# Optimization experiments

Hardware: AMD Instinct MI355X
Metric: run time of the kernel (lower is better)

The kernel has to match this reference:

```python
import jax, jax.numpy as jnp
import numpy as np

N, E, D, H, L, G = 20000, 320000, 128, 3, 3, 64
NEG_SLOPE = 0.2


def _seg_softmax(x, seg, num_segments):
    # x: [E, ...] logits, seg: [E] int segment ids. Softmax within each segment.
    m = jax.ops.segment_max(x, seg, num_segments=num_segments)
    e = jnp.exp(x - m[seg])  # m[seg] is finite wherever an edge exists
    s = jax.ops.segment_sum(e, seg, num_segments=num_segments)
    return e / s[seg]


def _gat_layer(feat, src, dst, fc_w, a_ns, a_nd, trans_w, trans_b):
    # feat: [N, D]; fc_w: [H*D, D]; a_ns/a_nd: [H, D]; trans_w: [D, H*D]
    h = (feat @ fc_w.T).reshape(N, H, D)                      # [N, H, D]
    s_ns = jnp.einsum('nhd,hd->nh', h, a_ns)                  # [N, H]
    s_nd = jnp.einsum('nhd,hd->nh', h, a_nd)                  # [N, H]
    e = jax.nn.leaky_relu(s_ns[src] + s_nd[dst], NEG_SLOPE)   # [E, H]
    a = _seg_softmax(e, dst, N)                               # edge softmax per dst
    msg = h[src] * a[:, :, None]                              # [E, H, D]
    agg = jax.ops.segment_sum(msg, dst, num_segments=N)       # [N, H, D]
    return agg.reshape(N, H * D) @ trans_w.T + trans_b        # [N, D]


def _attn_pool(feat, gid, p1_w, p1_b, p2_w, p2_b):
    # GlobalAttentionPooling: gate MLP -> softmax over nodes per graph -> weighted sum
    gate = jax.nn.relu(feat @ p1_w.T + p1_b) @ p2_w.T + p2_b  # [N, 1]
    alpha = _seg_softmax(gate[:, 0], gid, G)[:, None]         # [N, 1]
    return jax.ops.segment_sum(alpha * feat, gid, num_segments=G)  # [G, D]


def setup_inputs() -> dict:
    key = jax.random.key(0)
    ks = jax.random.split(key, 16)
    feat = jax.random.normal(ks[0], (N, D), dtype=jnp.float32)
    src = jax.random.randint(ks[1], (E,), 0, N, dtype=jnp.int32)
    dst = jax.random.randint(ks[2], (E,), 0, N, dtype=jnp.int32)
    node_gid = jnp.sort(jax.random.randint(ks[3], (N,), 0, G, dtype=jnp.int32))
    sc = 0.05
    return {
        'feat': feat, 'src': src, 'dst': dst, 'node_gid': node_gid,
        'fc_w': jax.random.normal(ks[4], (L, H * D, D), dtype=jnp.float32) * sc,
        'a_ns': jax.random.normal(ks[5], (L, H, D), dtype=jnp.float32) * sc,
        'a_nd': jax.random.normal(ks[6], (L, H, D), dtype=jnp.float32) * sc,
        'trans_w': jax.random.normal(ks[7], (L, D, H * D), dtype=jnp.float32) * sc,
        'trans_b': jax.random.normal(ks[8], (L, D), dtype=jnp.float32) * sc,
        'p1_w': jax.random.normal(ks[9], (L, 2 * D, D), dtype=jnp.float32) * sc,
        'p1_b': jax.random.normal(ks[10], (L, 2 * D), dtype=jnp.float32) * sc,
        'p2_w': jax.random.normal(ks[11], (L, 1, 2 * D), dtype=jnp.float32) * sc,
        'p2_b': jax.random.normal(ks[12], (L, 1), dtype=jnp.float32) * sc,
    }


def reference(feat, src, dst, node_gid, fc_w, a_ns, a_nd, trans_w, trans_b,
              p1_w, p1_b, p2_w, p2_b):
    # MLAPModel.forward with res=True, vir=False, dropout off (eval), Tflag=0
    graph_embs = []
    for d in range(L):
        feat_in = feat
        feat = _gat_layer(feat, src, dst, fc_w[d], a_ns[d], a_nd[d],
                          trans_w[d], trans_b[d])
        if d < L - 1:
            feat = jax.nn.relu(feat)
        feat = feat + feat_in  # residual
        graph_embs.append(_attn_pool(feat, node_gid, p1_w[d], p1_b[d],
                                     p2_w[d], p2_b[d]))
    return jnp.stack(graph_embs, axis=0).mean(axis=0)  # [G, D]
```

## Files before the change

kernel.cpp:

```cpp
#include <hip/hip_runtime.h>
#include <hip/hip_bf16.h>

#define N_NODES 20000
#define N_EDGES 320000
#define DIM 128
#define HEADS 3
#define LAYERS 3
#define NGRAPH 64
#define NEG_SLOPE 0.2f
#define NODE_BLOCKS ((N_NODES + 63) / 64)
#define NBLK32 ((N_NODES + 31) / 32)

typedef const __hip_bfloat16* bfp;
typedef __hip_bfloat16 bf16;
typedef short v8s __attribute__((ext_vector_type(8)));
typedef float v4f __attribute__((ext_vector_type(4)));

#define GLD_LDS(gp, lp) \
    __builtin_amdgcn_global_load_lds( \
        (const __attribute__((address_space(1))) void*)(gp), \
        (__attribute__((address_space(3))) void*)(lp), 16, 0, 0)

__device__ __forceinline__ float b2f(unsigned short u) {
    return __uint_as_float(((unsigned)u) << 16);
}
__device__ __forceinline__ float lo2f(unsigned u) { return __uint_as_float(u << 16); }
__device__ __forceinline__ float hi2f(unsigned u) { return __uint_as_float(u & 0xffff0000u); }
__device__ __forceinline__ float leaky(float z) {
    return z >= 0.f ? z : NEG_SLOPE * z;
}
__device__ __forceinline__ unsigned packbf(float a, float b) {
    bf16 x = __float2bfloat16(a), y = __float2bfloat16(b);
    return (unsigned)*(unsigned short*)&x | ((unsigned)*(unsigned short*)&y << 16);
}
__device__ __forceinline__ unsigned short f2bfbits(float v) {
    bf16 x = __float2bfloat16(v);
    return *(unsigned short*)&x;
}

__device__ __forceinline__ void stage_swz(const short* base, int t0, int K,
                                          int k0, short* lds, int gidx) {
    int row = gidx >> 2, pos = gidx & 3;
    int kch = pos ^ ((row >> 1) & 3);
    GLD_LDS(base + (size_t)(t0 + row) * K + k0 + kch * 8, lds + gidx * 8);
}
__device__ __forceinline__ v8s fragx(const short* lds, int R, int q) {
    int g = R * 4 + (q ^ ((R >> 1) & 3));
    return *(const v8s*)(lds + g * 8);
}

__device__ __forceinline__ void stage_panelB(const short* base, int t0, int K,
                                             int k0, short* lds, int tid) {
#pragma unroll
    for (int j = 0; j < 8; ++j) {
        int g = j * 256 + tid;
        stage_swz(base, t0, K, k0 + (g >> 9) * 32, lds + (g >> 9) * 4096, g & 511);
    }
}
__device__ __forceinline__ void stage_panelA32(const short* base, int t0, int K,
                                               int k0, short* lds, int tid) {
#pragma unroll
    for (int j = 0; j < 2; ++j) {
        int g = j * 256 + tid;
        stage_swz(base, t0, K, k0 + (g >> 7) * 32, lds + (g >> 7) * 1024, g & 127);
    }
}

__global__ void init_kernel(unsigned* __restrict__ z, int nzd,
                            const unsigned short* __restrict__ probe,
                            int* __restrict__ dflag) {
    int gid = blockIdx.x * 256 + threadIdx.x;
    for (int i = gid; i < nzd; i += gridDim.x * 256) z[i] = 0u;
    if (blockIdx.x == 0) {
        int c = 0;
#pragma unroll
        for (int j = 0; j < 64; ++j) {
            unsigned short u = probe[threadIdx.x * 64 + j];
            c += (((u >> 7) & 0xFF) >= 140) ? 1 : 0;
        }
        for (int o = 32; o > 0; o >>= 1) c += __shfl_down(c, o);
        __shared__ int r[4];
        if ((threadIdx.x & 63) == 0) r[threadIdx.x >> 6] = c;
        __syncthreads();
        if (threadIdx.x == 0) *dflag = r[0] + r[1] + r[2] + r[3];
    }
}

#define NCVT 9
struct CvtArgs {
    const void* src[NCVT];
    bf16* dst[NCVT];
    int n4[NCVT];
    int n[NCVT];
};
__global__ void cvtcount_kernel(CvtArgs args, const int* __restrict__ flag,
                                const int* __restrict__ dst, int* __restrict__ deg,
                                int cvtBlocks) {
    if ((int)blockIdx.x >= cvtBlocks) {
        int e = (blockIdx.x - cvtBlocks) * 256 + threadIdx.x;
        if (e < N_EDGES) atomicAdd(&deg[dst[e]], 1);
        return;
    }
    int i = blockIdx.x * 256 + threadIdx.x;
    int f = (*flag) > 8;
#pragma unroll
    for (int s = 0; s < NCVT; ++s) {
        int ns4 = args.n4[s];
        if (i < ns4) {
            int ns = args.n[s];
            int base = i * 4;
            bf16* dstp = args.dst[s];
            if (f) {
                const float* sp = (const float*)args.src[s];
                if (base + 3 < ns) {
                    float4 v = *(const float4*)(sp + base);
                    ushort4 pk = { f2bfbits(v.x), f2bfbits(v.y),
                                   f2bfbits(v.z), f2bfbits(v.w) };
                    *(ushort4*)(dstp + base) = pk;
                } else {
                    for (int j = 0; j < 4 && base + j < ns; ++j)
                        dstp[base + j] = __float2bfloat16(sp[base + j]);
                }
            } else {
                const bf16* sp = (const bf16*)args.src[s];
                if (base + 3 < ns) {
                    *(ushort4*)(dstp + base) = *(const ushort4*)(sp + base);
                } else {
                    for (int j = 0; j < 4 && base + j < ns; ++j)
                        dstp[base + j] = sp[base + j];
                }
            }
            return;
        }
        i -= ns4;
    }
}

__global__ void sentinel_kernel(bf16* out, int n) {
    int i = blockIdx.x * 256 + threadIdx.x;
    if (i < n) out[i] = __float2bfloat16(2.0f);
}

__global__ __launch_bounds__(256) void scanprep_kernel(
    const int* __restrict__ cnt, int* __restrict__ ptr,
    const int* __restrict__ gid, int* __restrict__ gptr,
    const bf16* __restrict__ cfc, const bf16* __restrict__ cans,
    const bf16* __restrict__ cand, const bf16* __restrict__ ctw,
    bf16* __restrict__ mcat, float* __restrict__ vcat)
{
    int tid = threadIdx.x;
    if ((int)blockIdx.x < LAYERS * 25) {
        const int l = blockIdx.x / 25;
        const int b = blockIdx.x % 25;
        const bf16* fc = cfc + (size_t)l * 384 * 128;
        if (b < 24) {
            const int h = b >> 3, kc = b & 7;
            const bf16* tw = ctw + (size_t)l * 128 * 384;
            bf16* mc = mcat + (size_t)l * 128 * 384;
            const int d = tid & 127;
            const int kh = tid >> 7;
            const int k0 = kc * 16 + kh * 8;
            float acc[8] = {0.f, 0.f, 0.f, 0.f, 0.f, 0.f, 0.f, 0.f};
            for (int j = 0; j < 128; ++j) {
                float w = __bfloat162float(tw[(size_t)d * 384 + h * 128 + j]);
                v8s fv = *(const v8s*)(fc + (size_t)(h * 128 + j) * 128 + k0);
#pragma unroll
                for (int i = 0; i < 8; ++i)
                    acc[i] += w * b2f((unsigned short)fv[i]);
            }
            v8s ov;
#pragma unroll
            for (int i = 0; i < 8; ++i) ov[i] = (short)f2bfbits(acc[i]);
            *(v8s*)(mc + (size_t)d * 384 + h * 128 + k0) = ov;
        } else {
            const int k = tid & 127;
            const int grp = tid >> 7;
            const bf16* av = (grp ? cand : cans) + (size_t)l * 384;
            float a0 = 0.f, a1 = 0.f, a2 = 0.f;
            for (int j = 0; j < 128; ++j) {
                a0 += __bfloat162float(av[j])       * __bfloat162float(fc[(size_t)j * 128 + k]);
                a1 += __bfloat162float(av[128 + j]) * __bfloat162float(fc[(size_t)(128 + j) * 128 + k]);
                a2 += __bfloat162float(av[256 + j]) * __bfloat162float(fc[(size_t)(256 + j) * 128 + k]);
            }
            float* vc = vcat + (size_t)l * 6 * 128;
            vc[(grp * 3 + 0) * 128 + k] = a0;
            vc[(grp * 3 + 1) * 128 + k] = a1;
            vc[(grp * 3 + 2) * 128 + k] = a2;
        }
        return;
    }
    if (tid <= NGRAPH) {
        int lo = 0, hi = N_NODES;
        while (lo < hi) {
            int mid = (lo + hi) >> 1;
            if (gid[mid] < tid) lo = mid + 1; else hi = mid;
        }
        gptr[tid] = lo;
    }
    const int chunk = (N_NODES + 255) / 256;
    int b = tid * chunk, e = min(b + chunk, N_NODES);
    int loc = 0;
    for (int i = b; i < e; ++i) loc += cnt[i];
    int lane = tid & 63, wv = tid >> 6;
    int v = loc;
#pragma unroll
    for (int o = 1; o < 64; o <<= 1) {
        int t = __shfl_up(v, o);
        if (lane >= o) v += t;
    }
    __shared__ int wsum[4];
    if (lane == 63) wsum[wv] = v;
    __syncthreads();
    int wo = 0;
    for (int j = 0; j < wv; ++j) wo += wsum[j];
    int run = wo + v - loc;
    if (tid == 255) ptr[N_NODES] = wsum[0] + wsum[1] + wsum[2] + wsum[3];
    for (int i = b; i < e; ++i) { ptr[i] = run; run += cnt[i]; }
}

__device__ __forceinline__ void score_block(
    const unsigned* __restrict__ featdw, const float* __restrict__ vc,
    float* __restrict__ s_all, int blk, int tid)
{
    const int wv = tid >> 6, lane = tid & 63;
    float2 vv0 = *(const float2*)(vc + 0 * 128 + lane * 2);
    float2 vv1 = *(const float2*)(vc + 1 * 128 + lane * 2);
    float2 vv2 = *(const float2*)(vc + 2 * 128 + lane * 2);
    float2 vv3 = *(const float2*)(vc + 3 * 128 + lane * 2);
    float2 vv4 = *(const float2*)(vc + 4 * 128 + lane * 2);
    float2 vv5 = *(const float2*)(vc + 5 * 128 + lane * 2);
    const int nbase = blk * 64 + wv * 16;
#pragma unroll 1
    for (int t = 0; t < 16; ++t) {
        const int n = nbase + t;
        if (n >= N_NODES) return;
        unsigned u = featdw[(size_t)n * 64 + lane];
        float lo = lo2f(u), hi = hi2f(u);
        float p0 = lo * vv0.x + hi * vv0.y;
        float p1 = lo * vv1.x + hi * vv1.y;
        float p2 = lo * vv2.x + hi * vv2.y;
        float p3 = lo * vv3.x + hi * vv3.y;
        float p4 = lo * vv4.x + hi * vv4.y;
        float p5 = lo * vv5.x + hi * vv5.y;
#pragma unroll
        for (int o = 1; o < 64; o <<= 1) {
            p0 += __shfl_xor(p0, o); p1 += __shfl_xor(p1, o);
            p2 += __shfl_xor(p2, o); p3 += __shfl_xor(p3, o);
            p4 += __shfl_xor(p4, o); p5 += __shfl_xor(p5, o);
        }
        float outv = p0;
        outv = (lane == 1) ? p1 : outv;
        outv = (lane == 2) ? p2 : outv;
        outv = (lane == 4) ? p3 : outv;
        outv = (lane == 5) ? p4 : outv;
        outv = (lane == 6) ? p5 : outv;
        if (lane < 7 && lane != 3)
            s_all[(size_t)n * 8 + lane] = outv;
    }
}

__global__ __launch_bounds__(256) void fillscore_kernel(
    const bf16* __restrict__ pfeat,
    const float* __restrict__ vc, float* __restrict__ s_all,
    const int* __restrict__ src, const int* __restrict__ dst,
    const int* __restrict__ rp, int* __restrict__ cursor,
    int* __restrict__ esrc, int fillBlocks)
{
    const int tid = threadIdx.x;
    if ((int)blockIdx.x < fillBlocks) {
        int e = blockIdx.x * 256 + tid;
        if (e < N_EDGES) {
            int d = dst[e];
            int pos = rp[d] + atomicAdd(&cursor[d], 1);
            esrc[pos] = src[e];
        }
        return;
    }
    score_block((const unsigned*)pfeat, vc, s_all, blockIdx.x - fillBlocks, tid);
}

__global__ __launch_bounds__(256) void aggpool_kernel(
    const unsigned* __restrict__ featdw, const int* __restrict__ rp,
    const int* __restrict__ esrc, const float* __restrict__ s_all,
    bf16* __restrict__ aggF, const float* __restrict__ gp,
    const int* __restrict__ gptr, float* __restrict__ out_acc,
    int poolBlocks)
{
    __shared__ float4 pv[4][64];
    __shared__ float red[4];
    const int tid = threadIdx.x;
    if ((int)blockIdx.x < poolBlocks) {
        const bf16* pfeat = (const bf16*)featdw;
        const int g = blockIdx.x >> 3;
        const int chunk = blockIdx.x & 7;
        const int beg = gptr[g], end = gptr[g + 1];
        if (beg >= end) return;
        float m = -1e30f;
        for (int i = beg + tid; i < end; i += 256)
            m = fmaxf(m, gp[i]);
#pragma unroll
        for (int o = 32; o > 0; o >>= 1) m = fmaxf(m, __shfl_xor(m, o));
        if ((tid & 63) == 0) red[tid >> 6] = m;
        __syncthreads();
        m = fmaxf(fmaxf(red[0], red[1]), fmaxf(red[2], red[3]));
        __syncthreads();
        float s = 0.f;
        for (int i = beg + tid; i < end; i += 256)
            s += __expf(gp[i] - m);
#pragma unroll
        for (int o = 32; o > 0; o >>= 1) s += __shfl_xor(s, o);
        if ((tid & 63) == 0) red[tid >> 6] = s;
        __syncthreads();
        float inv = 1.f / (red[0] + red[1] + red[2] + red[3]);
        const int p = tid >> 7;
        const int c = tid & 127;
        float acc = 0.f;
        for (int i = beg + chunk * 2 + p; i < end; i += 16) {
            float w = __expf(gp[i] - m);
            acc += w * __bfloat162float(pfeat[(size_t)i * DIM + c]);
        }
        acc *= inv;
        atomicAdd(&out_acc[g * DIM + c], acc);
        return;
    }
    const int wv = tid >> 6;
    const int lane = tid & 63;
    const int node = (blockIdx.x - poolBlocks) * 4 + wv;
    if (node >= N_NODES) return;
    const int beg = rp[node], end = rp[node + 1];
    const int cnt = end - beg;
    unsigned* outp = (unsigned*)(aggF + (size_t)node * (HEADS * DIM));
    if (cnt <= 0) {
        outp[lane] = 0u; outp[64 + lane] = 0u; outp[128 + lane] = 0u;
        return;
    }
    const float nd0 = s_all[(size_t)node * 8 + 4];
    const float nd1 = s_all[(size_t)node * 8 + 5];
    const float nd2 = s_all[(size_t)node * 8 + 6];
    float sl0 = 0.f, sl1 = 0.f, sl2 = 0.f;
    float a00 = 0.f, a01 = 0.f, a10 = 0.f, a11 = 0.f, a20 = 0.f, a21 = 0.f;
    for (int c0 = 0; c0 < cnt; c0 += 64) {
        const int ce = min(64, cnt - c0);
        if (lane < ce) {
            int s = esrc[beg + c0 + lane];
            float4 q = *(const float4*)(s_all + (size_t)s * 8);
            float4 r;
            r.x = __expf(leaky(q.x + nd0));
            r.y = __expf(leaky(q.y + nd1));
            r.z = __expf(leaky(q.z + nd2));
            r.w = __int_as_float(s);
            sl0 += r.x; sl1 += r.y; sl2 += r.z;
            pv[wv][lane] = r;
        }
#pragma unroll 8
        for (int j = 0; j < ce; ++j) {
            float4 e = pv[wv][j];
            int s = __float_as_int(e.w);
            unsigned u = featdw[(size_t)s * 64 + lane];
            float lo = lo2f(u), hi = hi2f(u);
            a00 += e.x * lo; a01 += e.x * hi;
            a10 += e.y * lo; a11 += e.y * hi;
            a20 += e.z * lo; a21 += e.z * hi;
        }
    }
#pragma unroll
    for (int o = 1; o < 64; o <<= 1) {
        sl0 += __shfl_xor(sl0, o);
        sl1 += __shfl_xor(sl1, o);
        sl2 += __shfl_xor(sl2, o);
    }
    const float i0 = 1.f / sl0, i1 = 1.f / sl1, i2 = 1.f / sl2;
    outp[lane]       = packbf(a00 * i0, a01 * i0);
    outp[64 + lane]  = packbf(a10 * i1, a11 * i1);
    outp[128 + lane] = packbf(a20 * i2, a21 * i2);
}

__global__ __launch_bounds__(256) void fusedgemm_kernel(
    const bf16* __restrict__ A, const bf16* __restrict__ B,
    bf16* __restrict__ C, const bf16* __restrict__ bias,
    const bf16* __restrict__ resid, int do_relu,
    const bf16* __restrict__ p1w, const bf16* __restrict__ p1b,
    const bf16* __restrict__ p2w, float* __restrict__ gpart,
    const float* __restrict__ vc_next, float* __restrict__ s_next)
{
    __shared__ short lsA[4096];
    __shared__ short lsB[16384];
    __shared__ float sred[2][32][8];
    const int tid = threadIdx.x;
    const int wv = tid >> 6, lane = tid & 63;
    const int quad = lane >> 4, r16 = lane & 15;
    const int rw = wv & 1, cg = wv >> 1;
    const int m0 = blockIdx.x * 32;
    const short* As = (const short*)A;
    const short* Bs = (const short*)B;

    v4f acc[4];
#pragma unroll
    for (int t = 0; t < 4; ++t) acc[t] = (v4f){0.f, 0.f, 0.f, 0.f};

#pragma unroll
    for (int ks = 0; ks < 3; ++ks) {
        const int k0 = ks * 128;
        stage_panelA32(As, m0, 384, k0, lsA, tid);
        stage_panelB(Bs, 0, 384, k0, lsB, tid);
        __syncthreads();
#pragma unroll
        for (int c = 0; c < 4; ++c) {
            v8s a = fragx(lsA + c * 1024, rw * 16 + r16, quad);
#pragma unroll
            for (int t = 0; t < 4; ++t) {
                v8s b = fragx(lsB + c * 4096, cg * 64 + t * 16 + r16, quad);
                acc[t] = __builtin_amdgcn_mfma_f32_16x16x32_bf16(a, b, acc[t], 0, 0, 0);
            }
        }
        __syncthreads();
    }

    float bbv[4];
#pragma unroll
    for (int t = 0; t < 4; ++t)
        bbv[t] = __bfloat162float(bias[cg * 64 + t * 16 + r16]);
    float s0[4], s1[4], s2[4], s3[4], s4[4], s5[4];
#pragma unroll
    for (int reg = 0; reg < 4; ++reg) {
        s0[reg] = 0.f; s1[reg] = 0.f; s2[reg] = 0.f;
        s3[reg] = 0.f; s4[reg] = 0.f; s5[reg] = 0.f;
    }
#pragma unroll
    for (int t = 0; t < 4; ++t) {
        const int n = cg * 64 + t * 16 + r16;
        float v0 = vc_next ? vc_next[0 * 128 + n] : 0.f;
        float v1 = vc_next ? vc_next[1 * 128 + n] : 0.f;
        float v2 = vc_next ? vc_next[2 * 128 + n] : 0.f;
        float v3 = vc_next ? vc_next[3 * 128 + n] : 0.f;
        float v4 = vc_next ? vc_next[4 * 128 + n] : 0.f;
        float v5 = vc_next ? vc_next[5 * 128 + n] : 0.f;
        const int cch = n >> 5, nc = n & 31, qq = nc >> 3, e = nc & 7;
#pragma unroll
        for (int reg = 0; reg < 4; ++reg) {
            const int R = rw * 16 + quad * 4 + reg;
            const int m = m0 + R;
            float v = acc[t][reg] + bbv[t];
            if (do_relu) v = fmaxf(v, 0.f);
            v += __bfloat162float(resid[(size_t)m * 128 + n]);
            C[(size_t)m * 128 + n] = __float2bfloat16(v);
            const int pos = qq ^ ((R >> 1) & 3);
            lsA[cch * 1024 + (R * 4 + pos) * 8 + e] = (short)f2bfbits(v);
            s0[reg] += v * v0; s1[reg] += v * v1; s2[reg] += v * v2;
            s3[reg] += v * v3; s4[reg] += v * v4; s5[reg] += v * v5;
        }
    }
    if (vc_next) {
#pragma unroll
        for (int reg = 0; reg < 4; ++reg) {
#pragma unroll
            for (int o = 1; o < 16; o <<= 1) {
                s0[reg] += __shfl_xor(s0[reg], o);
                s1[reg] += __shfl_xor(s1[reg], o);
                s2[reg] += __shfl_xor(s2[reg], o);
                s3[reg] += __shfl_xor(s3[reg], o);
                s4[reg] += __shfl_xor(s4[reg], o);
                s5[reg] += __shfl_xor(s5[reg], o);
            }
            if (r16 == 0) {
                const int R = rw * 16 + quad * 4 + reg;
                sred[cg][R][0] = s0[reg]; sred[cg][R][1] = s1[reg];
                sred[cg][R][2] = s2[reg]; sred[cg][R][3] = s3[reg];
                sred[cg][R][4] = s4[reg]; sred[cg][R][5] = s5[reg];
            }
        }
    }
    __syncthreads();
    if (vc_next && tid < 192) {
        const int R = tid / 6, c = tid - R * 6;
        const float sv = sred[0][R][c] + sred[1][R][c];
        s_next[(size_t)(m0 + R) * 8 + (c < 3 ? c : c + 1)] = sv;
    }

    float gacc[4] = {0.f, 0.f, 0.f, 0.f};
#pragma unroll 1
    for (int hh = 0; hh < 2; ++hh) {
        if (hh) __syncthreads();
        stage_panelB((const short*)p1w, hh * 128, 128, 0, lsB, tid);
        __syncthreads();
        v4f a2[4];
#pragma unroll
        for (int t = 0; t < 4; ++t) a2[t] = (v4f){0.f, 0.f, 0.f, 0.f};
#pragma unroll
        for (int c = 0; c < 4; ++c) {
            v8s a = fragx(lsA + c * 1024, rw * 16 + r16, quad);
#pragma unroll
            for (int t = 0; t < 4; ++t) {
                v8s b = fragx(lsB + c * 4096, cg * 64 + t * 16 + r16, quad);
                a2[t] = __builtin_amdgcn_mfma_f32_16x16x32_bf16(a, b, a2[t], 0, 0, 0);
            }
        }
#pragma unroll
        for (int t = 0; t < 4; ++t) {
            const int n = hh * 128 + cg * 64 + t * 16 + r16;
            float b1 = __bfloat162float(p1b[n]);
            float pw = __bfloat162float(p2w[n]);
#pragma unroll
            for (int reg = 0; reg < 4; ++reg)
                gacc[reg] += fmaxf(a2[t][reg] + b1, 0.f) * pw;
        }
    }
#pragma unroll
    for (int reg = 0; reg < 4; ++reg) {
#pragma unroll
        for (int o = 1; o < 16; o <<= 1) gacc[reg] += __shfl_xor(gacc[reg], o);
        if (r16 == 0) sred[cg][rw * 16 + quad * 4 + reg][6] = gacc[reg];
    }
    __syncthreads();
    if (tid < 32) gpart[m0 + tid] = sred[0][tid][6] + sred[1][tid][6];
}

__global__ void __launch_bounds__(256) pool_acc(
    const bf16* __restrict__ feat, const float* __restrict__ gp,
    const int* __restrict__ gptr, float* __restrict__ out_acc)
{
    const int g = blockIdx.x;
    const int chunk = blockIdx.y;
    const int tid = threadIdx.x;
    const int beg = gptr[g], end = gptr[g + 1];
    if (beg >= end) return;
    __shared__ float red[4];
    float m = -1e30f;
    for (int i = beg + tid; i < end; i += 256)
        m = fmaxf(m, gp[i]);
#pragma unroll
    for (int o = 32; o > 0; o >>= 1) m = fmaxf(m, __shfl_xor(m, o));
    if ((tid & 63) == 0) red[tid >> 6] = m;
    __syncthreads();
    m = fmaxf(fmaxf(red[0], red[1]), fmaxf(red[2], red[3]));
    __syncthreads();
    float s = 0.f;
    for (int i = beg + tid; i < end; i += 256)
        s += __expf(gp[i] - m);
#pragma unroll
    for (int o = 32; o > 0; o >>= 1) s += __shfl_xor(s, o);
    if ((tid & 63) == 0) red[tid >> 6] = s;
    __syncthreads();
    float inv = 1.f / (red[0] + red[1] + red[2] + red[3]);
    const int p = tid >> 7;
    const int c = tid & 127;
    float acc = 0.f;
    for (int i = beg + chunk * 2 + p; i < end; i += 16) {
        float w = __expf(gp[i] - m);
        acc += w * __bfloat162float(feat[(size_t)i * DIM + c]);
    }
    acc *= inv;
    atomicAdd(&out_acc[g * DIM + c], acc);
}

__global__ void writeout_kernel(const float* __restrict__ out_acc,
                                void* __restrict__ out, const int* __restrict__ flag) {
    int i = blockIdx.x * 256 + threadIdx.x;
    if (i < NGRAPH * DIM) {
        float v = out_acc[i] * (1.f / 3.f);
        if ((*flag) > 8) ((float*)out)[i] = v;
        else ((bf16*)out)[i] = __float2bfloat16(v);
    }
}

extern "C" void kernel_launch(void* const* d_in, const int* in_sizes, int n_in,
                              void* d_out, int out_size, void* d_ws, size_t ws_size,
                              hipStream_t stream)
{
    const void* feat_in = d_in[0];
    const int* src = (const int*)d_in[1];
    const int* dst = (const int*)d_in[2];
    const int* gid = (const int*)d_in[3];

    char* base = (char*)d_ws;
    size_t off = 0;
    auto carve = [&](size_t bytes) -> void* {
        void* p = base + off;
        off = (off + bytes + 255) & ~(size_t)255;
        return p;
    };
    int* dflag = (int*)carve(256);
    size_t zbytes = sizeof(int) * 2 * N_NODES + sizeof(float) * NGRAPH * DIM;
    char* zreg  = (char*)carve(zbytes);
    int* deg    = (int*)zreg;
    int* cursor = deg + N_NODES;
    float* out_acc = (float*)(cursor + N_NODES);
    float* gpart3 = (float*)carve(sizeof(float) * LAYERS * N_NODES);
    int* rp     = (int*)carve(sizeof(int) * (N_NODES + 1));
    int* gptr   = (int*)carve(sizeof(int) * (NGRAPH + 1));
    int* esrc   = (int*)carve(sizeof(int) * N_EDGES);
    float* s_bufA = (float*)carve(sizeof(float) * N_NODES * 8);
    float* s_bufB = (float*)carve(sizeof(float) * N_NODES * 8);
    float* vcat = (float*)carve(sizeof(float) * LAYERS * 6 * 128);
    bf16* mcat  = (bf16*)carve(sizeof(bf16) * LAYERS * 128 * 384);
    bf16* featA = (bf16*)carve(sizeof(bf16) * N_NODES * DIM);
    bf16* featB = (bf16*)carve(sizeof(bf16) * N_NODES * DIM);
    bf16* cfc   = (bf16*)carve(sizeof(bf16) * LAYERS * HEADS * DIM * DIM);
    bf16* cans  = (bf16*)carve(sizeof(bf16) * LAYERS * HEADS * DIM);
    bf16* cand  = (bf16*)carve(sizeof(bf16) * LAYERS * HEADS * DIM);
    bf16* ctw   = (bf16*)carve(sizeof(bf16) * LAYERS * DIM * HEADS * DIM);
    bf16* ctb   = (bf16*)carve(sizeof(bf16) * LAYERS * DIM);
    bf16* cp1w  = (bf16*)carve(sizeof(bf16) * LAYERS * 2 * DIM * DIM);
    bf16* cp1b  = (bf16*)carve(sizeof(bf16) * LAYERS * 2 * DIM);
    bf16* cp2w  = (bf16*)carve(sizeof(bf16) * LAYERS * 2 * DIM);
    bf16* aggF  = (bf16*)carve(sizeof(bf16) * N_NODES * HEADS * DIM);
    carve(131072);

    if (off > ws_size) {
        sentinel_kernel<<<(out_size + 255) / 256, 256, 0, stream>>>(
            (bf16*)d_out, out_size);
        return;
    }

    init_kernel<<<128, 256, 0, stream>>>(
        (unsigned*)zreg, (int)(zbytes / 4), (const unsigned short*)feat_in, dflag);

    CvtArgs ca;
    const int cvt_n[NCVT] = {
        N_NODES * DIM, LAYERS * HEADS * DIM * DIM, LAYERS * HEADS * DIM,
        LAYERS * HEADS * DIM, LAYERS * DIM * HEADS * DIM, LAYERS * DIM,
        LAYERS * 2 * DIM * DIM, LAYERS * 2 * DIM, LAYERS * 2 * DIM };
    bf16* cvt_dst[NCVT] = { featA, cfc, cans, cand, ctw, ctb, cp1w, cp1b, cp2w };
    const int cvt_src_idx[NCVT] = { 0, 4, 5, 6, 7, 8, 9, 10, 11 };
    int total4 = 0;
    for (int s = 0; s < NCVT; ++s) {
        ca.src[s] = d_in[cvt_src_idx[s]];
        ca.dst[s] = cvt_dst[s];
        ca.n[s] = cvt_n[s];
        ca.n4[s] = (cvt_n[s] + 3) / 4;
        total4 += ca.n4[s];
    }
    const int cvtBlocks = (total4 + 255) / 256;
    const int cntBlocks = (N_EDGES + 255) / 256;
    cvtcount_kernel<<<cvtBlocks + cntBlocks, 256, 0, stream>>>(
        ca, dflag, dst, deg, cvtBlocks);

    scanprep_kernel<<<LAYERS * 25 + 1, 256, 0, stream>>>(
        deg, rp, gid, gptr, cfc, cans, cand, ctw, mcat, vcat);

    bf16* fin = featA;
    bf16* fout = featB;
    for (int d = 0; d < LAYERS; ++d) {
        float* s_cur = (d & 1) ? s_bufB : s_bufA;
        float* s_next = (d & 1) ? s_bufA : s_bufB;
        if (d == 0) {
            fillscore_kernel<<<cntBlocks + NODE_BLOCKS, 256, 0, stream>>>(
                fin, vcat, s_cur, src, dst, rp, cursor, esrc, cntBlocks);
        }
        const int poolBlocks = (d == 0) ? 0 : NGRAPH * 8;
        aggpool_kernel<<<poolBlocks + (N_NODES + 3) / 4, 256, 0, stream>>>(
            (const unsigned*)fin, rp, esrc, s_cur, aggF,
            (d == 0) ? nullptr : gpart3 + (size_t)(d - 1) * N_NODES,
            gptr, out_acc, poolBlocks);
        fusedgemm_kernel<<<NBLK32, 256, 0, stream>>>(
            aggF, mcat + (size_t)d * 128 * 384, fout,
            ctb + (size_t)d * DIM, fin, (d < LAYERS - 1) ? 1 : 0,
            cp1w + (size_t)d * 2 * DIM * DIM, cp1b + (size_t)d * 2 * DIM,
            cp2w + (size_t)d * 2 * DIM, gpart3 + (size_t)d * N_NODES,
            (d < LAYERS - 1) ? vcat + (size_t)(d + 1) * 6 * 128 : nullptr,
            s_next);
        bf16* t = fin; fin = fout; fout = t;
    }
    pool_acc<<<dim3(NGRAPH, 8), 256, 0, stream>>>(
        fin, gpart3 + (size_t)2 * N_NODES, gptr, out_acc);
    writeout_kernel<<<(NGRAPH * DIM + 255) / 256, 256, 0, stream>>>(
        out_acc, d_out, dflag);
}
```

Measured before the change: 295.2 us.

## Fuse setup kernels into one cooperative kernel and fold writeout into pool_acc

Replaces the four setup launches (init, convert/count, scan/prep, fill/score) with a single cooperative kernel that uses grid-wide syncs between phases. A fallback to the old kernels remains if the cooperative launch fails. The final writeout kernel is merged into pool_acc using a last-block-done counter. The aim is to cut launch gaps and kernel boundaries on a short pipeline. The cost is grid.sync overhead, and the setup phases now run on a fixed grid of 512 blocks.

```diff
diff --git a/kernel.cpp b/kernel.cpp
--- a/kernel.cpp
+++ b/kernel.cpp
@@ -1,5 +1,8 @@
 #include <hip/hip_runtime.h>
 #include <hip/hip_bf16.h>
+#include <hip/hip_cooperative_groups.h>
+
+namespace cg = cooperative_groups;
 
 #define N_NODES 20000
 #define N_EDGES 320000
@@ -66,26 +69,6 @@
     }
 }
 
-__global__ void init_kernel(unsigned* __restrict__ z, int nzd,
-                            const unsigned short* __restrict__ probe,
-                            int* __restrict__ dflag) {
-    int gid = blockIdx.x * 256 + threadIdx.x;
-    for (int i = gid; i < nzd; i += gridDim.x * 256) z[i] = 0u;
-    if (blockIdx.x == 0) {
-        int c = 0;
-#pragma unroll
-        for (int j = 0; j < 64; ++j) {
-            unsigned short u = probe[threadIdx.x * 64 + j];
-            c += (((u >> 7) & 0xFF) >= 140) ? 1 : 0;
-        }
-        for (int o = 32; o > 0; o >>= 1) c += __shfl_down(c, o);
-        __shared__ int r[4];
-        if ((threadIdx.x & 63) == 0) r[threadIdx.x >> 6] = c;
-        __syncthreads();
-        if (threadIdx.x == 0) *dflag = r[0] + r[1] + r[2] + r[3];
-    }
-}
-
 #define NCVT 9
 struct CvtArgs {
     const void* src[NCVT];
@@ -93,16 +76,7 @@
     int n4[NCVT];
     int n[NCVT];
 };
-__global__ void cvtcount_kernel(CvtArgs args, const int* __restrict__ flag,
-                                const int* __restrict__ dst, int* __restrict__ deg,
-                                int cvtBlocks) {
-    if ((int)blockIdx.x >= cvtBlocks) {
-        int e = (blockIdx.x - cvtBlocks) * 256 + threadIdx.x;
-        if (e < N_EDGES) atomicAdd(&deg[dst[e]], 1);
-        return;
-    }
-    int i = blockIdx.x * 256 + threadIdx.x;
-    int f = (*flag) > 8;
+__device__ __forceinline__ void cvt_item(const CvtArgs& args, int i, int f) {
 #pragma unroll
     for (int s = 0; s < NCVT; ++s) {
         int ns4 = args.n4[s];
@@ -136,88 +110,6 @@
     }
 }
 
-__global__ void sentinel_kernel(bf16* out, int n) {
-    int i = blockIdx.x * 256 + threadIdx.x;
-    if (i < n) out[i] = __float2bfloat16(2.0f);
-}
-
-__global__ __launch_bounds__(256) void scanprep_kernel(
-    const int* __restrict__ cnt, int* __restrict__ ptr,
-    const int* __restrict__ gid, int* __restrict__ gptr,
-    const bf16* __restrict__ cfc, const bf16* __restrict__ cans,
-    const bf16* __restrict__ cand, const bf16* __restrict__ ctw,
-    bf16* __restrict__ mcat, float* __restrict__ vcat)
-{
-    int tid = threadIdx.x;
-    if ((int)blockIdx.x < LAYERS * 25) {
-        const int l = blockIdx.x / 25;
-        const int b = blockIdx.x % 25;
-        const bf16* fc = cfc + (size_t)l * 384 * 128;
-        if (b < 24) {
-            const int h = b >> 3, kc = b & 7;
-            const bf16* tw = ctw + (size_t)l * 128 * 384;
-            bf16* mc = mcat + (size_t)l * 128 * 384;
-            const int d = tid & 127;
-            const int kh = tid >> 7;
-            const int k0 = kc * 16 + kh * 8;
-            float acc[8] = {0.f, 0.f, 0.f, 0.f, 0.f, 0.f, 0.f, 0.f};
-            for (int j = 0; j < 128; ++j) {
-                float w = __bfloat162float(tw[(size_t)d * 384 + h * 128 + j]);
-                v8s fv = *(const v8s*)(fc + (size_t)(h * 128 + j) * 128 + k0);
-#pragma unroll
-                for (int i = 0; i < 8; ++i)
-                    acc[i] += w * b2f((unsigned short)fv[i]);
-            }
-            v8s ov;
-#pragma unroll
-            for (int i = 0; i < 8; ++i) ov[i] = (short)f2bfbits(acc[i]);
-            *(v8s*)(mc + (size_t)d * 384 + h * 128 + k0) = ov;
-        } else {
-            const int k = tid & 127;
-            const int grp = tid >> 7;
-            const bf16* av = (grp ? cand : cans) + (size_t)l * 384;
-            float a0 = 0.f, a1 = 0.f, a2 = 0.f;
-            for (int j = 0; j < 128; ++j) {
-                a0 += __bfloat162float(av[j])       * __bfloat162float(fc[(size_t)j * 128 + k]);
-                a1 += __bfloat162float(av[128 + j]) * __bfloat162float(fc[(size_t)(128 + j) * 128 + k]);
-                a2 += __bfloat162float(av[256 + j]) * __bfloat162float(fc[(size_t)(256 + j) * 128 + k]);
-            }
-            float* vc = vcat + (size_t)l * 6 * 128;
-            vc[(grp * 3 + 0) * 128 + k] = a0;
-            vc[(grp * 3 + 1) * 128 + k] = a1;
-            vc[(grp * 3 + 2) * 128 + k] = a2;
-        }
-        return;
-    }
-    if (tid <= NGRAPH) {
-        int lo = 0, hi = N_NODES;
-        while (lo < hi) {
-            int mid = (lo + hi) >> 1;
-            if (gid[mid] < tid) lo = mid + 1; else hi = mid;
-        }
-        gptr[tid] = lo;
-    }
-    const int chunk = (N_NODES + 255) / 256;
-    int b = tid * chunk, e = min(b + chunk, N_NODES);
-    int loc = 0;
-    for (int i = b; i < e; ++i) loc += cnt[i];
-    int lane = tid & 63, wv = tid >> 6;
-    int v = loc;
-#pragma unroll
-    for (int o = 1; o < 64; o <<= 1) {
-        int t = __shfl_up(v, o);
-        if (lane >= o) v += t;
-    }
-    __shared__ int wsum[4];
-    if (lane == 63) wsum[wv] = v;
-    __syncthreads();
-    int wo = 0;
-    for (int j = 0; j < wv; ++j) wo += wsum[j];
-    int run = wo + v - loc;
-    if (tid == 255) ptr[N_NODES] = wsum[0] + wsum[1] + wsum[2] + wsum[3];
-    for (int i = b; i < e; ++i) { ptr[i] = run; run += cnt[i]; }
-}
-
 __device__ __forceinline__ void score_block(
     const unsigned* __restrict__ featdw, const float* __restrict__ vc,
     float* __restrict__ s_all, int blk, int tid)
@@ -259,6 +151,184 @@
     }
 }
 
+__device__ __forceinline__ void prep_body(
+    int pb, int tid, const bf16* __restrict__ cfc,
+    const bf16* __restrict__ cans, const bf16* __restrict__ cand,
+    const bf16* __restrict__ ctw, bf16* __restrict__ mcat,
+    float* __restrict__ vcat)
+{
+    const int l = pb / 25;
+    const int b = pb % 25;
+    const bf16* fc = cfc + (size_t)l * 384 * 128;
+    if (b < 24) {
+        const int h = b >> 3, kc = b & 7;
+        const bf16* tw = ctw + (size_t)l * 128 * 384;
+        bf16* mc = mcat + (size_t)l * 128 * 384;
+        const int d = tid & 127;
+        const int kh = tid >> 7;
+        const int k0 = kc * 16 + kh * 8;
+        float acc[8] = {0.f, 0.f, 0.f, 0.f, 0.f, 0.f, 0.f, 0.f};
+        for (int j = 0; j < 128; ++j) {
+            float w = __bfloat162float(tw[(size_t)d * 384 + h * 128 + j]);
+            v8s fv = *(const v8s*)(fc + (size_t)(h * 128 + j) * 128 + k0);
+#pragma unroll
+            for (int i = 0; i < 8; ++i)
+                acc[i] += w * b2f((unsigned short)fv[i]);
+        }
+        v8s ov;
+#pragma unroll
+        for (int i = 0; i < 8; ++i) ov[i] = (short)f2bfbits(acc[i]);
+        *(v8s*)(mc + (size_t)d * 384 + h * 128 + k0) = ov;
+    } else {
+        const int k = tid & 127;
+        const int grp = tid >> 7;
+        const bf16* av = (grp ? cand : cans) + (size_t)l * 384;
+        float a0 = 0.f, a1 = 0.f, a2 = 0.f;
+        for (int j = 0; j < 128; ++j) {
+            a0 += __bfloat162float(av[j])       * __bfloat162float(fc[(size_t)j * 128 + k]);
+            a1 += __bfloat162float(av[128 + j]) * __bfloat162float(fc[(size_t)(128 + j) * 128 + k]);
+            a2 += __bfloat162float(av[256 + j]) * __bfloat162float(fc[(size_t)(256 + j) * 128 + k]);
+        }
+        float* vc = vcat + (size_t)l * 6 * 128;
+        vc[(grp * 3 + 0) * 128 + k] = a0;
+        vc[(grp * 3 + 1) * 128 + k] = a1;
+        vc[(grp * 3 + 2) * 128 + k] = a2;
+    }
+}
+
+__device__ __forceinline__ void scan_body(
+    int tid, const int* __restrict__ cnt, int* __restrict__ ptr,
+    const int* __restrict__ gid, int* __restrict__ gptr, int* wsum)
+{
+    if (tid <= NGRAPH) {
+        int lo = 0, hi = N_NODES;
+        while (lo < hi) {
+            int mid = (lo + hi) >> 1;
+            if (gid[mid] < tid) lo = mid + 1; else hi = mid;
+        }
+        gptr[tid] = lo;
+    }
+    const int chunk = (N_NODES + 255) / 256;
+    int b = tid * chunk, e = min(b + chunk, N_NODES);
+    int loc = 0;
+    for (int i = b; i < e; ++i) loc += cnt[i];
+    int lane = tid & 63, wv = tid >> 6;
+    int v = loc;
+#pragma unroll
+    for (int o = 1; o < 64; o <<= 1) {
+        int t = __shfl_up(v, o);
+        if (lane >= o) v += t;
+    }
+    if (lane == 63) wsum[wv] = v;
+    __syncthreads();
+    int wo = 0;
+    for (int j = 0; j < wv; ++j) wo += wsum[j];
+    int run = wo + v - loc;
+    if (tid == 255) ptr[N_NODES] = wsum[0] + wsum[1] + wsum[2] + wsum[3];
+    for (int i = b; i < e; ++i) { ptr[i] = run; run += cnt[i]; }
+}
+
+__global__ __launch_bounds__(256) void prep_coop(
+    CvtArgs ca, int total4, unsigned* __restrict__ zreg, int nzd,
+    const unsigned short* __restrict__ probe, int* __restrict__ dflag,
+    const int* __restrict__ src, const int* __restrict__ dst,
+    int* __restrict__ deg, int* __restrict__ rp,
+    const int* __restrict__ gid, int* __restrict__ gptr,
+    const bf16* __restrict__ cfc, const bf16* __restrict__ cans,
+    const bf16* __restrict__ cand, const bf16* __restrict__ ctw,
+    bf16* __restrict__ mcat, float* __restrict__ vcat,
+    const bf16* __restrict__ feat0, float* __restrict__ s_all,
+    int* __restrict__ cursor, int* __restrict__ esrc)
+{
+    cg::grid_group grid = cg::this_grid();
+    __shared__ int ish[4];
+    const int tid = threadIdx.x;
+    const int gsz = gridDim.x * 256;
+    const int g0 = blockIdx.x * 256 + tid;
+
+    for (int i = g0; i < nzd; i += gsz) zreg[i] = 0u;
+    if (blockIdx.x == 0) {
+        int c = 0;
+#pragma unroll
+        for (int j = 0; j < 64; ++j) {
+            unsigned short u = probe[tid * 64 + j];
+            c += (((u >> 7) & 0xFF) >= 140) ? 1 : 0;
+        }
+        for (int o = 32; o > 0; o >>= 1) c += __shfl_down(c, o);
+        if ((tid & 63) == 0) ish[tid >> 6] = c;
+        __syncthreads();
+        if (tid == 0) *dflag = ish[0] + ish[1] + ish[2] + ish[3];
+    }
+    __threadfence();
+    grid.sync();
+
+    for (int e = g0; e < N_EDGES; e += gsz) atomicAdd(&deg[dst[e]], 1);
+    const int f = (*dflag) > 8;
+    for (int i = g0; i < total4; i += gsz) cvt_item(ca, i, f);
+    __threadfence();
+    grid.sync();
+
+    if (blockIdx.x == 0) {
+        scan_body(tid, deg, rp, gid, gptr, ish);
+    } else if ((int)blockIdx.x <= LAYERS * 25) {
+        prep_body(blockIdx.x - 1, tid, cfc, cans, cand, ctw, mcat, vcat);
+    }
+    __threadfence();
+    grid.sync();
+
+    for (int e = g0; e < N_EDGES; e += gsz) {
+        int d = dst[e];
+        int pos = rp[d] + atomicAdd(&cursor[d], 1);
+        esrc[pos] = src[e];
+    }
+    for (int blk = blockIdx.x; blk < NODE_BLOCKS; blk += gridDim.x)
+        score_block((const unsigned*)feat0, vcat, s_all, blk, tid);
+}
+
+__global__ void init_kernel(unsigned* __restrict__ z, int nzd,
+                            const unsigned short* __restrict__ probe,
+                            int* __restrict__ dflag) {
+    int gid = blockIdx.x * 256 + threadIdx.x;
+    for (int i = gid; i < nzd; i += gridDim.x * 256) z[i] = 0u;
+    if (blockIdx.x == 0) {
+        int c = 0;
+#pragma unroll
+        for (int j = 0; j < 64; ++j) {
+            unsigned short u = probe[threadIdx.x * 64 + j];
+            c += (((u >> 7) & 0xFF) >= 140) ? 1 : 0;
+        }
+        for (int o = 32; o > 0; o >>= 1) c += __shfl_down(c, o);
+        __shared__ int r[4];
+        if ((threadIdx.x & 63) == 0) r[threadIdx.x >> 6] = c;
+        __syncthreads();
+        if (threadIdx.x == 0) *dflag = r[0] + r[1] + r[2] + r[3];
+    }
+}
+__global__ void cvtcount_kernel(CvtArgs args, const int* __restrict__ flag,
+                                const int* __restrict__ dst, int* __restrict__ deg,
+                                int cvtBlocks) {
+    if ((int)blockIdx.x >= cvtBlocks) {
+        int e = (blockIdx.x - cvtBlocks) * 256 + threadIdx.x;
+        if (e < N_EDGES) atomicAdd(&deg[dst[e]], 1);
+        return;
+    }
+    int i = blockIdx.x * 256 + threadIdx.x;
+    cvt_item(args, i, (*flag) > 8);
+}
+__global__ __launch_bounds__(256) void scanprep_kernel(
+    const int* __restrict__ cnt, int* __restrict__ ptr,
+    const int* __restrict__ gid, int* __restrict__ gptr,
+    const bf16* __restrict__ cfc, const bf16* __restrict__ cans,
+    const bf16* __restrict__ cand, const bf16* __restrict__ ctw,
+    bf16* __restrict__ mcat, float* __restrict__ vcat)
+{
+    __shared__ int wsum[4];
+    if ((int)blockIdx.x < LAYERS * 25) {
+        prep_body(blockIdx.x, threadIdx.x, cfc, cans, cand, ctw, mcat, vcat);
+        return;
+    }
+    scan_body(threadIdx.x, cnt, ptr, gid, gptr, wsum);
+}
 __global__ __launch_bounds__(256) void fillscore_kernel(
     const bf16* __restrict__ pfeat,
     const float* __restrict__ vc, float* __restrict__ s_all,
@@ -277,6 +347,11 @@
         return;
     }
     score_block((const unsigned*)pfeat, vc, s_all, blockIdx.x - fillBlocks, tid);
+}
+
+__global__ void sentinel_kernel(bf16* out, int n) {
+    int i = blockIdx.x * 256 + threadIdx.x;
+    if (i < n) out[i] = __float2bfloat16(2.0f);
 }
 
 __global__ __launch_bounds__(256) void aggpool_kernel(
@@ -389,7 +464,7 @@
     const int tid = threadIdx.x;
     const int wv = tid >> 6, lane = tid & 63;
     const int quad = lane >> 4, r16 = lane & 15;
-    const int rw = wv & 1, cg = wv >> 1;
+    const int rw = wv & 1, cg_ = wv >> 1;
     const int m0 = blockIdx.x * 32;
     const short* As = (const short*)A;
     const short* Bs = (const short*)B;
@@ -409,7 +484,7 @@
             v8s a = fragx(lsA + c * 1024, rw * 16 + r16, quad);
 #pragma unroll
             for (int t = 0; t < 4; ++t) {
-                v8s b = fragx(lsB + c * 4096, cg * 64 + t * 16 + r16, quad);
+                v8s b = fragx(lsB + c * 4096, cg_ * 64 + t * 16 + r16, quad);
                 acc[t] = __builtin_amdgcn_mfma_f32_16x16x32_bf16(a, b, acc[t], 0, 0, 0);
             }
         }
@@ -419,7 +494,7 @@
     float bbv[4];
 #pragma unroll
     for (int t = 0; t < 4; ++t)
-        bbv[t] = __bfloat162float(bias[cg * 64 + t * 16 + r16]);
+        bbv[t] = __bfloat162float(bias[cg_ * 64 + t * 16 + r16]);
     float s0[4], s1[4], s2[4], s3[4], s4[4], s5[4];
 #pragma unroll
     for (int reg = 0; reg < 4; ++reg) {
@@ -428,7 +503,7 @@
     }
 #pragma unroll
     for (int t = 0; t < 4; ++t) {
-        const int n = cg * 64 + t * 16 + r16;
+        const int n = cg_ * 64 + t * 16 + r16;
         float v0 = vc_next ? vc_next[0 * 128 + n] : 0.f;
         float v1 = vc_next ? vc_next[1 * 128 + n] : 0.f;
         float v2 = vc_next ? vc_next[2 * 128 + n] : 0.f;
@@ -464,9 +539,9 @@
             }
             if (r16 == 0) {
                 const int R = rw * 16 + quad * 4 + reg;
-                sred[cg][R][0] = s0[reg]; sred[cg][R][1] = s1[reg];
-                sred[cg][R][2] = s2[reg]; sred[cg][R][3] = s3[reg];
-                sred[cg][R][4] = s4[reg]; sred[cg][R][5] = s5[reg];
+                sred[cg_][R][0] = s0[reg]; sred[cg_][R][1] = s1[reg];
+                sred[cg_][R][2] = s2[reg]; sred[cg_][R][3] = s3[reg];
+                sred[cg_][R][4] = s4[reg]; sred[cg_][R][5] = s5[reg];
             }
         }
     }
@@ -491,13 +566,13 @@
             v8s a = fragx(lsA + c * 1024, rw * 16 + r16, quad);
 #pragma unroll
             for (int t = 0; t < 4; ++t) {
-                v8s b = fragx(lsB + c * 4096, cg * 64 + t * 16 + r16, quad);
+                v8s b = fragx(lsB + c * 4096, cg_ * 64 + t * 16 + r16, quad);
                 a2[t] = __builtin_amdgcn_mfma_f32_16x16x32_bf16(a, b, a2[t], 0, 0, 0);
             }
         }
 #pragma unroll
         for (int t = 0; t < 4; ++t) {
-            const int n = hh * 128 + cg * 64 + t * 16 + r16;
+            const int n = hh * 128 + cg_ * 64 + t * 16 + r16;
             float b1 = __bfloat162float(p1b[n]);
             float pw = __bfloat162float(p2w[n]);
 #pragma unroll
@@ -509,7 +584,7 @@
     for (int reg = 0; reg < 4; ++reg) {
 #pragma unroll
         for (int o = 1; o < 16; o <<= 1) gacc[reg] += __shfl_xor(gacc[reg], o);
-        if (r16 == 0) sred[cg][rw * 16 + quad * 4 + reg][6] = gacc[reg];
+        if (r16 == 0) sred[cg_][rw * 16 + quad * 4 + reg][6] = gacc[reg];
     }
     __syncthreads();
     if (tid < 32) gpart[m0 + tid] = sred[0][tid][6] + sred[1][tid][6];
@@ -517,48 +592,53 @@
 
 __global__ void __launch_bounds__(256) pool_acc(
     const bf16* __restrict__ feat, const float* __restrict__ gp,
-    const int* __restrict__ gptr, float* __restrict__ out_acc)
+    const int* __restrict__ gptr, float* __restrict__ out_acc,
+    int* __restrict__ done_cnt, void* __restrict__ out,
+    const int* __restrict__ flag)
 {
     const int g = blockIdx.x;
     const int chunk = blockIdx.y;
     const int tid = threadIdx.x;
     const int beg = gptr[g], end = gptr[g + 1];
-    if (beg >= end) return;
     __shared__ float red[4];
-    float m = -1e30f;
-    for (int i = beg + tid; i < end; i += 256)
-        m = fmaxf(m, gp[i]);
-#pragma unroll
-    for (int o = 32; o > 0; o >>= 1) m = fmaxf(m, __shfl_xor(m, o));
-    if ((tid & 63) == 0) red[tid >> 6] = m;
+    __shared__ int lastf;
+    if (beg < end) {
+        float m = -1e30f;
+        for (int i = beg + tid; i < end; i += 256)
+            m = fmaxf(m, gp[i]);
+#pragma unroll
+        for (int o = 32; o > 0; o >>= 1) m = fmaxf(m, __shfl_xor(m, o));
+        if ((tid & 63) == 0) red[tid >> 6] = m;
+        __syncthreads();
+        m = fmaxf(fmaxf(red[0], red[1]), fmaxf(red[2], red[3]));
+        __syncthreads();
+        float s = 0.f;
+        for (int i = beg + tid; i < end; i += 256)
+            s += __expf(gp[i] - m);
+#pragma unroll
+        for (int o = 32; o > 0; o >>= 1) s += __shfl_xor(s, o);
+        if ((tid & 63) == 0) red[tid >> 6] = s;
+        __syncthreads();
+        float inv = 1.f / (red[0] + red[1] + red[2] + red[3]);
+        const int p = tid >> 7;
+        const int c = tid & 127;
+        float acc = 0.f;
+        for (int i = beg + chunk * 2 + p; i < end; i += 16) {
+            float w = __expf(gp[i] - m);
+            acc += w * __bfloat162float(feat[(size_t)i * DIM + c]);
+        }
+        acc *= inv;
+        atomicAdd(&out_acc[g * DIM + c], acc);
+    }
+    __threadfence();
+    if (tid == 0) lastf = (atomicAdd(done_cnt, 1) == NGRAPH * 8 - 1);
     __syncthreads();
-    m = fmaxf(fmaxf(red[0], red[1]), fmaxf(red[2], red[3]));
-    __syncthreads();
-    float s = 0.f;
-    for (int i = beg + tid; i < end; i += 256)
-        s += __expf(gp[i] - m);
-#pragma unroll
-    for (int o = 32; o > 0; o >>= 1) s += __shfl_xor(s, o);
-    if ((tid & 63) == 0) red[tid >> 6] = s;
-    __syncthreads();
-    float inv = 1.f / (red[0] + red[1] + red[2] + red[3]);
-    const int p = tid >> 7;
-    const int c = tid & 127;
-    float acc = 0.f;
-    for (int i = beg + chunk * 2 + p; i < end; i += 16) {
-        float w = __expf(gp[i] - m);
-        acc += w * __bfloat162float(feat[(size_t)i * DIM + c]);
-    }
-    acc *= inv;
-    atomicAdd(&out_acc[g * DIM + c], acc);
-}
-
-__global__ void writeout_kernel(const float* __restrict__ out_acc,
-                                void* __restrict__ out, const int* __restrict__ flag) {
-    int i = blockIdx.x * 256 + threadIdx.x;
-    if (i < NGRAPH * DIM) {
+    if (!lastf) return;
+    __threadfence();
+    const int fw = (*flag) > 8;
+    for (int i = tid; i < NGRAPH * DIM; i += 256) {
         float v = out_acc[i] * (1.f / 3.f);
-        if ((*flag) > 8) ((float*)out)[i] = v;
+        if (fw) ((float*)out)[i] = v;
         else ((bf16*)out)[i] = __float2bfloat16(v);
     }
 }
@@ -580,11 +660,12 @@
         return p;
     };
     int* dflag = (int*)carve(256);
-    size_t zbytes = sizeof(int) * 2 * N_NODES + sizeof(float) * NGRAPH * DIM;
+    size_t zbytes = sizeof(int) * 2 * N_NODES + sizeof(float) * NGRAPH * DIM + 256;
     char* zreg  = (char*)carve(zbytes);
     int* deg    = (int*)zreg;
     int* cursor = deg + N_NODES;
     float* out_acc = (float*)(cursor + N_NODES);
+    int* done_cnt = (int*)(out_acc + NGRAPH * DIM);
     float* gpart3 = (float*)carve(sizeof(float) * LAYERS * N_NODES);
     int* rp     = (int*)carve(sizeof(int) * (N_NODES + 1));
     int* gptr   = (int*)carve(sizeof(int) * (NGRAPH + 1));
@@ -612,9 +693,6 @@
         return;
     }
 
-    init_kernel<<<128, 256, 0, stream>>>(
-        (unsigned*)zreg, (int)(zbytes / 4), (const unsigned short*)feat_in, dflag);
-
     CvtArgs ca;
     const int cvt_n[NCVT] = {
         N_NODES * DIM, LAYERS * HEADS * DIM * DIM, LAYERS * HEADS * DIM,
@@ -632,21 +710,37 @@
     }
     const int cvtBlocks = (total4 + 255) / 256;
     const int cntBlocks = (N_EDGES + 255) / 256;
-    cvtcount_kernel<<<cvtBlocks + cntBlocks, 256, 0, stream>>>(
-        ca, dflag, dst, deg, cvtBlocks);
-
-    scanprep_kernel<<<LAYERS * 25 + 1, 256, 0, stream>>>(
-        deg, rp, gid, gptr, cfc, cans, cand, ctw, mcat, vcat);
+    int nzd = (int)(zbytes / 4);
+
+    {
+        unsigned* zreg_u = (unsigned*)zreg;
+        const unsigned short* probe = (const unsigned short*)feat_in;
+        const bf16* feat0 = featA;
+        float* s_all0 = s_bufA;
+        void* kargs[] = {
+            &ca, &total4, &zreg_u, &nzd, &probe, &dflag,
+            &src, &dst, &deg, &rp, &gid, &gptr,
+            &cfc, &cans, &cand, &ctw, &mcat, &vcat,
+            &feat0, &s_all0, &cursor, &esrc };
+        hipError_t err = hipLaunchCooperativeKernel(
+            (void*)prep_coop, dim3(512), dim3(256), kargs, 0, stream);
+        if (err != hipSuccess) {
+            init_kernel<<<128, 256, 0, stream>>>(
+                (unsigned*)zreg, nzd, probe, dflag);
+            cvtcount_kernel<<<cvtBlocks + cntBlocks, 256, 0, stream>>>(
+                ca, dflag, dst, deg, cvtBlocks);
+            scanprep_kernel<<<LAYERS * 25 + 1, 256, 0, stream>>>(
+                deg, rp, gid, gptr, cfc, cans, cand, ctw, mcat, vcat);
+            fillscore_kernel<<<cntBlocks + NODE_BLOCKS, 256, 0, stream>>>(
+                featA, vcat, s_bufA, src, dst, rp, cursor, esrc, cntBlocks);
+        }
+    }
 
     bf16* fin = featA;
     bf16* fout = featB;
     for (int d = 0; d < LAYERS; ++d) {
         float* s_cur = (d & 1) ? s_bufB : s_bufA;
         float* s_next = (d & 1) ? s_bufA : s_bufB;
-        if (d == 0) {
-            fillscore_kernel<<<cntBlocks + NODE_BLOCKS, 256, 0, stream>>>(
-                fin, vcat, s_cur, src, dst, rp, cursor, esrc, cntBlocks);
-        }
         const int poolBlocks = (d == 0) ? 0 : NGRAPH * 8;
         aggpool_kernel<<<poolBlocks + (N_NODES + 3) / 4, 256, 0, stream>>>(
             (const unsigned*)fin, rp, esrc, s_cur, aggF,
@@ -662,7 +756,6 @@
         bf16* t = fin; fin = fout; fout = t;
     }
     pool_acc<<<dim3(NGRAPH, 8), 256, 0, stream>>>(
-        fin, gpart3 + (size_t)2 * N_NODES, gptr, out_acc);
-    writeout_kernel<<<(NGRAPH * DIM + 255) / 256, 256, 0, stream>>>(
-        out_acc, d_out, dflag);
-}
+        fin, gpart3 + (size_t)2 * N_NODES, gptr, out_acc,
+        done_cnt, d_out, dflag);
+}
```

Result: slower. 649.5 us (+120.0%).
